# Optimization experiments

Hardware: AMD Instinct MI355X
Metric: run time of the kernel (lower is better)

## Reference

```python
import jax, jax.numpy as jnp
import numpy as np

D_K, D_V, H, N = 128, 256, 256, 50
B, L = 128, 1024

def setup_inputs() -> dict:
    key = jax.random.key(0)
    ks = jax.random.split(key, 10)
    s = lambda fan_in: 1.0 / np.sqrt(fan_in)
    return {
        'problems': jax.random.normal(ks[0], (B, L, D_K), dtype=jnp.float32),
        'interactions': jax.random.normal(ks[1], (B, L, D_V), dtype=jnp.float32),
        'w_key': jax.random.uniform(ks[2], (N, D_K), jnp.float32, -s(D_K), s(D_K)),
        'w_erase_w': jax.random.uniform(ks[3], (D_V, D_V), jnp.float32, -s(D_V), s(D_V)),
        'w_erase_b': jax.random.uniform(ks[4], (D_V,), jnp.float32, -s(D_V), s(D_V)),
        'w_add_w': jax.random.uniform(ks[5], (D_V, D_V), jnp.float32, -s(D_V), s(D_V)),
        'w_add_b': jax.random.uniform(ks[6], (D_V,), jnp.float32, -s(D_V), s(D_V)),
        'w_out_w': jax.random.uniform(ks[7], (H, D_V + D_K), jnp.float32, -s(D_V + D_K), s(D_V + D_K)),
        'w_out_b': jax.random.uniform(ks[8], (H,), jnp.float32, -s(D_V + D_K), s(D_V + D_K)),
        'init_memory': jax.random.normal(ks[9], (N, D_V), dtype=jnp.float32),
    }

def reference(problems, interactions, w_key, w_erase_w, w_erase_b, w_add_w, w_add_b, w_out_w, w_out_b, init_memory):
    # Precompute per-step gates outside the scan (they do not depend on memory)
    e = jax.nn.sigmoid(jnp.einsum('bld,ed->ble', interactions, w_erase_w) + w_erase_b)  # (B,L,d_v)
    a = jnp.tanh(jnp.einsum('bld,ed->ble', interactions, w_add_w) + w_add_b)            # (B,L,d_v)
    score = jax.nn.softmax(jnp.einsum('bld,nd->bln', problems, w_key), axis=-1)          # (B,L,n)

    mem0 = jnp.broadcast_to(init_memory, (problems.shape[0], N, D_V))

    def step(memory, xs):
        sc_t, e_t, a_t = xs  # (B,n), (B,d_v), (B,d_v)
        read = jnp.einsum('bn,bnd->bd', sc_t, memory)  # weighted read
        memory = memory * (1.0 - sc_t[:, :, None] * e_t[:, None, :])
        memory = memory + sc_t[:, :, None] * a_t[:, None, :]
        return memory, read

    xs = (score.transpose(1, 0, 2), e.transpose(1, 0, 2), a.transpose(1, 0, 2))  # time-major
    _, reads = jax.lax.scan(step, mem0, xs)  # reads: (L,B,d_v)

    x = jnp.concatenate([reads.transpose(1, 0, 2), problems], axis=-1)  # (B,L,d_v+d_k)
    # dropout in eval mode = identity
    return jnp.tanh(jnp.einsum('blc,hc->blh', x, w_out_w) + w_out_b)
```

## Files before the change

### kernel.cpp

```cpp
#include <hip/hip_runtime.h>

#define B_    128
#define L_    1024
#define DK_   128
#define DV_   256
#define NS_   50
#define H_    256
#define M_    (B_ * L_)

typedef __attribute__((ext_vector_type(8))) short   short8;
typedef __attribute__((ext_vector_type(4))) float   float4v;
typedef __attribute__((ext_vector_type(4))) int     int4v;

__device__ __forceinline__ float b2f(unsigned short u) {
    unsigned int x = ((unsigned int)u) << 16;
    return __builtin_bit_cast(float, x);
}
__device__ __forceinline__ unsigned short f2b(float f) {
    unsigned int x = __builtin_bit_cast(unsigned int, f);
    x += 0x7fffu + ((x >> 16) & 1u);
    return (unsigned short)(x >> 16);
}
__device__ __forceinline__ int pack2(float lo, float hi) {
    return (int)f2b(lo) | ((int)f2b(hi) << 16);
}
__device__ __forceinline__ float sigmoid_f(float x) {
    return 1.f / (1.f + __expf(-x));
}
__device__ __forceinline__ float tanh_f(float x) {
    return 1.f - 2.f / (__expf(2.f * x) + 1.f);
}

__device__ __forceinline__ void gload_lds16(const void* g, void* l) {
    __builtin_amdgcn_global_load_lds(
        (const __attribute__((address_space(1))) void*)g,
        (__attribute__((address_space(3))) void*)l, 16, 0, 0);
}

__global__ __launch_bounds__(256) void gate_kernel(
    const float* __restrict__ X,
    const float* __restrict__ We, const float* __restrict__ be,
    const float* __restrict__ Wa, const float* __restrict__ ba,
    unsigned short* __restrict__ e_out, unsigned short* __restrict__ a_out)
{
    constexpr int K = DV_;
    const int mblk = blockIdx.x, nblk = blockIdx.y, gate = blockIdx.z;
    const float* W    = gate ? Wa : We;
    const float* bias = gate ? ba : be;
    unsigned short* out = gate ? a_out : e_out;

    __shared__ unsigned short As[128 * 40];
    __shared__ unsigned short Bs[128 * 40];

    const int tid  = threadIdx.x;
    const int lane = tid & 63, wid = tid >> 6;
    const int wm = wid >> 1, wn = wid & 1;
    const int l15 = lane & 15, quad = lane >> 4;

    float4v acc[4][4];
#pragma unroll
    for (int i = 0; i < 4; i++)
#pragma unroll
        for (int j = 0; j < 4; j++) {
            acc[i][j][0] = 0.f; acc[i][j][1] = 0.f;
            acc[i][j][2] = 0.f; acc[i][j][3] = 0.f;
        }

    const int srow = tid >> 1;
    const int scol = (tid & 1) * 16;
    const size_t Abase = ((size_t)mblk * 128 + srow) * K;
    const size_t Bbase = ((size_t)nblk * 128 + srow) * K;

    for (int k0 = 0; k0 < K; k0 += 32) {
        const float* xa = &X[Abase + k0 + scol];
        const float* xb = &W[Bbase + k0 + scol];
        int4v pa0, pa1, pb0, pb1;
#pragma unroll
        for (int j = 0; j < 4; j++) {
            pa0[j] = pack2(xa[2*j],     xa[2*j + 1]);
            pa1[j] = pack2(xa[2*j + 8], xa[2*j + 9]);
            pb0[j] = pack2(xb[2*j],     xb[2*j + 1]);
            pb1[j] = pack2(xb[2*j + 8], xb[2*j + 9]);
        }
        *(int4v*)&As[srow * 40 + scol]     = pa0;
        *(int4v*)&As[srow * 40 + scol + 8] = pa1;
        *(int4v*)&Bs[srow * 40 + scol]     = pb0;
        *(int4v*)&Bs[srow * 40 + scol + 8] = pb1;
        __syncthreads();
        short8 af[4], bf[4];
#pragma unroll
        for (int i = 0; i < 4; i++)
            af[i] = *(const short8*)&As[(64 * wm + 16 * i + l15) * 40 + quad * 8];
#pragma unroll
        for (int j = 0; j < 4; j++)
            bf[j] = *(const short8*)&Bs[(64 * wn + 16 * j + l15) * 40 + quad * 8];
#pragma unroll
        for (int i = 0; i < 4; i++)
#pragma unroll
            for (int j = 0; j < 4; j++)
                acc[i][j] = __builtin_amdgcn_mfma_f32_16x16x32_bf16(af[i], bf[j], acc[i][j], 0, 0, 0);
        __syncthreads();
    }

#pragma unroll
    for (int i = 0; i < 4; i++) {
        const int row = mblk * 128 + 64 * wm + 16 * i + quad * 4;
#pragma unroll
        for (int j = 0; j < 4; j++) {
            const int col = nblk * 128 + 64 * wn + 16 * j + l15;
            const float bv = bias[col];
#pragma unroll
            for (int r = 0; r < 4; r++) {
                float v = acc[i][j][r] + bv;
                v = gate ? tanh_f(v) : sigmoid_f(v);
                out[(size_t)(row + r) * DV_ + col] = f2b(v);
            }
        }
    }
}

__global__ __launch_bounds__(256) void score_kernel(
    const float* __restrict__ problems,
    const float* __restrict__ w_key,
    float* __restrict__ score_scan)
{
    const int rowi = blockIdx.x * 256 + threadIdx.x;
    const float* p = problems + (size_t)rowi * DK_;

    float logit[NS_];
#pragma unroll
    for (int n = 0; n < NS_; n++) logit[n] = 0.f;

    for (int k0 = 0; k0 < DK_; k0 += 4) {
        float pf0 = p[k0], pf1 = p[k0+1], pf2 = p[k0+2], pf3 = p[k0+3];
#pragma unroll
        for (int n = 0; n < NS_; n++) {
            const float* wk = &w_key[n * DK_ + k0];
            logit[n] += pf0 * wk[0] + pf1 * wk[1] + pf2 * wk[2] + pf3 * wk[3];
        }
    }

    float mx = logit[0];
#pragma unroll
    for (int n = 1; n < NS_; n++) mx = fmaxf(mx, logit[n]);
    float sum = 0.f;
#pragma unroll
    for (int n = 0; n < NS_; n++) { logit[n] = __expf(logit[n] - mx); sum += logit[n]; }
    const float inv = 1.f / sum;

    float* o = score_scan + (size_t)rowi * 64;
#pragma unroll
    for (int v = 0; v < 16; v++) {
        float4v st;
#pragma unroll
        for (int c = 0; c < 4; c++) {
            const int j  = v * 4 + c;
            const int ng = j >> 4, ii = j & 15;
            const int n  = ng * 13 + ii;
            st[c] = (ii < 13 && n < NS_) ? logit[n] * inv : 0.f;
        }
        *(float4v*)(o + v * 4) = st;
    }
}

#define TCH 64
#define NCH (L_ / TCH)

__global__ __launch_bounds__(256) void scan_kernel(
    const float* __restrict__ score_scan,
    const unsigned short* __restrict__ e_buf,
    const unsigned short* __restrict__ a_buf,
    const float* __restrict__ init_mem,
    unsigned short* __restrict__ reads)
{
    __shared__ float          score_s[2][TCH][64];
    __shared__ unsigned short e_s[2][TCH][64];
    __shared__ unsigned short a_s[2][TCH][64];

    const int b    = blockIdx.y;
    const int dblk = blockIdx.x;
    const int tid  = threadIdx.x;
    const int w    = tid >> 6;
    const int lane = tid & 63;
    const int dsub = lane & 15;
    const int ng   = lane >> 4;
    const int d    = dblk * 64 + w * 16 + dsub;

    float M[13];
#pragma unroll
    for (int i = 0; i < 13; i++) {
        const int n = ng * 13 + i;
        M[i] = (n < NS_) ? init_mem[n * DV_ + d] : 0.f;
    }

    const size_t rb = (size_t)b * L_;
    const int l4  = lane >> 4;
    const int c16 = lane & 15;
    const int l8  = lane >> 3;
    const int c8  = lane & 7;

    auto stage = [&](int c, int p) {
        const int t0 = c * TCH + w * 16;
#pragma unroll
        for (int i = 0; i < 4; i++) {
            const int tt = t0 + i * 4 + l4;
            gload_lds16(score_scan + ((rb + tt) * 64 + c16 * 4),
                        &score_s[p][w * 16 + i * 4][0]);
        }
#pragma unroll
        for (int i = 0; i < 2; i++) {
            const int tt = t0 + i * 8 + l8;
            gload_lds16(e_buf + ((rb + tt) * DV_ + dblk * 64 + c8 * 8),
                        &e_s[p][w * 16 + i * 8][0]);
            gload_lds16(a_buf + ((rb + tt) * DV_ + dblk * 64 + c8 * 8),
                        &a_s[p][w * 16 + i * 8][0]);
        }
    };

    unsigned short* rp = reads + rb * DV_ + d;

    int p = 0;
    stage(0, 0);
    asm volatile("s_waitcnt vmcnt(0)" ::: "memory");
    __syncthreads();

    for (int c = 0; c < NCH; ++c) {
        if (c + 1 < NCH) stage(c + 1, p ^ 1);

#pragma unroll 2
        for (int tt = 0; tt < TCH; ++tt) {
            const float* sc = &score_s[p][tt][ng * 16];
            const float4v s0 = *(const float4v*)(sc);
            const float4v s1 = *(const float4v*)(sc + 4);
            const float4v s2 = *(const float4v*)(sc + 8);
            const float   s3 = sc[12];
            const float e_cur = b2f(e_s[p][tt][w * 16 + dsub]);
            const float a_cur = b2f(a_s[p][tt][w * 16 + dsub]);

            float r = 0.f;
            const float sarr[13] = { s0[0], s0[1], s0[2], s0[3],
                                     s1[0], s1[1], s1[2], s1[3],
                                     s2[0], s2[1], s2[2], s2[3], s3 };
#pragma unroll
            for (int i = 0; i < 13; i++) {
                const float s = sarr[i];
                r = fmaf(s, M[i], r);
                M[i] = fmaf(s, fmaf(-e_cur, M[i], a_cur), M[i]);
            }
            r += __shfl_xor(r, 16);
            r += __shfl_xor(r, 32);
            if (ng == 0) rp[(size_t)(c * TCH + tt) * DV_] = f2b(r);
        }

        asm volatile("s_waitcnt vmcnt(0)" ::: "memory");
        __syncthreads();
        p ^= 1;
    }
}

__global__ __launch_bounds__(256) void out_kernel(
    const unsigned short* __restrict__ reads,
    const float* __restrict__ problems,
    const float* __restrict__ Wo,
    const float* __restrict__ bo,
    float* __restrict__ out)
{
    constexpr int K = DV_ + DK_;
    const int mblk = blockIdx.x, nblk = blockIdx.y;

    __shared__ unsigned short As[128 * 40];
    __shared__ unsigned short Bs[128 * 40];

    const int tid  = threadIdx.x;
    const int lane = tid & 63, wid = tid >> 6;
    const int wm = wid >> 1, wn = wid & 1;
    const int l15 = lane & 15, quad = lane >> 4;

    float4v acc[4][4];
#pragma unroll
    for (int i = 0; i < 4; i++)
#pragma unroll
        for (int j = 0; j < 4; j++) {
            acc[i][j][0] = 0.f; acc[i][j][1] = 0.f;
            acc[i][j][2] = 0.f; acc[i][j][3] = 0.f;
        }

    const int srow = tid >> 1;
    const int scol = (tid & 1) * 16;
    const size_t mrow = (size_t)mblk * 128 + srow;
    const size_t brow = (size_t)nblk * 128 + srow;

    for (int k0 = 0; k0 < K; k0 += 32) {
        const int kk = k0 + scol;
        int4v a0, a1;
        if (kk < DV_) {
            a0 = *(const int4v*)&reads[mrow * DV_ + kk];
            a1 = *(const int4v*)&reads[mrow * DV_ + kk + 8];
        } else {
            const float* pr = &problems[mrow * DK_ + (kk - DV_)];
#pragma unroll
            for (int j = 0; j < 4; j++) {
                a0[j] = pack2(pr[2*j],     pr[2*j + 1]);
                a1[j] = pack2(pr[2*j + 8], pr[2*j + 9]);
            }
        }
        const float* wb = &Wo[brow * K + kk];
        int4v b0, b1;
#pragma unroll
        for (int j = 0; j < 4; j++) {
            b0[j] = pack2(wb[2*j],     wb[2*j + 1]);
            b1[j] = pack2(wb[2*j + 8], wb[2*j + 9]);
        }
        *(int4v*)&As[srow * 40 + scol]     = a0;
        *(int4v*)&As[srow * 40 + scol + 8] = a1;
        *(int4v*)&Bs[srow * 40 + scol]     = b0;
        *(int4v*)&Bs[srow * 40 + scol + 8] = b1;
        __syncthreads();
        short8 af[4], bf[4];
#pragma unroll
        for (int i = 0; i < 4; i++)
            af[i] = *(const short8*)&As[(64 * wm + 16 * i + l15) * 40 + quad * 8];
#pragma unroll
        for (int j = 0; j < 4; j++)
            bf[j] = *(const short8*)&Bs[(64 * wn + 16 * j + l15) * 40 + quad * 8];
#pragma unroll
        for (int i = 0; i < 4; i++)
#pragma unroll
            for (int j = 0; j < 4; j++)
                acc[i][j] = __builtin_amdgcn_mfma_f32_16x16x32_bf16(af[i], bf[j], acc[i][j], 0, 0, 0);
        __syncthreads();
    }

#pragma unroll
    for (int i = 0; i < 4; i++) {
        const int row = mblk * 128 + 64 * wm + 16 * i + quad * 4;
#pragma unroll
        for (int j = 0; j < 4; j++) {
            const int col = nblk * 128 + 64 * wn + 16 * j + l15;
            const float bv = bo[col];
#pragma unroll
            for (int r = 0; r < 4; r++) {
                out[(size_t)(row + r) * H_ + col] = tanh_f(acc[i][j][r] + bv);
            }
        }
    }
}

extern "C" void kernel_launch(void* const* d_in, const int* in_sizes, int n_in,
                              void* d_out, int out_size, void* d_ws, size_t ws_size,
                              hipStream_t stream) {
    const float* problems  = (const float*)d_in[0];
    const float* interact  = (const float*)d_in[1];
    const float* w_key     = (const float*)d_in[2];
    const float* w_erase_w = (const float*)d_in[3];
    const float* w_erase_b = (const float*)d_in[4];
    const float* w_add_w   = (const float*)d_in[5];
    const float* w_add_b   = (const float*)d_in[6];
    const float* w_out_w   = (const float*)d_in[7];
    const float* w_out_b   = (const float*)d_in[8];
    const float* init_mem  = (const float*)d_in[9];

    char* ws = (char*)d_ws;
    const size_t SZ_BF = (size_t)M_ * DV_ * 2;
    unsigned short* e_buf = (unsigned short*)(ws);
    unsigned short* a_buf = (unsigned short*)(ws + SZ_BF);
    unsigned short* reads = (unsigned short*)(ws + 2 * SZ_BF);
    float*     score_scan = (float*)(ws + 3 * SZ_BF);

    gate_kernel<<<dim3(M_ / 128, DV_ / 128, 2), 256, 0, stream>>>(
        interact, w_erase_w, w_erase_b, w_add_w, w_add_b, e_buf, a_buf);

    score_kernel<<<M_ / 256, 256, 0, stream>>>(problems, w_key, score_scan);

    scan_kernel<<<dim3(4, B_), 256, 0, stream>>>(
        score_scan, e_buf, a_buf, init_mem, reads);

    out_kernel<<<dim3(M_ / 128, H_ / 128), 256, 0, stream>>>(
        reads, problems, w_out_w, w_out_b, (float*)d_out);
}
```

Before: 838.3 us.

## Repartition scan across more blocks with 8 slots per lane group

The recurrent scan kernel now assigns 32 memory columns per block instead of 64, doubling the grid to 8x128 blocks, and splits the 50 memory slots into groups of 8 per lane (with an extra shuffle reduction) instead of 13. The score layout is changed to a contiguous 64-wide padded vector to match, the time chunk shrinks to 32 steps, and launch bounds request 4 blocks per CU. The GEMM kernels also switch from scalar float loads to float4 vector loads before bf16 packing. The aim is more parallelism and occupancy in the latency-bound sequential scan, at the cost of an extra cross-lane reduction and more redundant score loading per block.

```diff
diff --git a/kernel.cpp b/kernel.cpp
--- a/kernel.cpp
+++ b/kernel.cpp
@@ -74,14 +74,23 @@
     for (int k0 = 0; k0 < K; k0 += 32) {
         const float* xa = &X[Abase + k0 + scol];
         const float* xb = &W[Bbase + k0 + scol];
+        float4v va0 = *(const float4v*)(xa);
+        float4v va1 = *(const float4v*)(xa + 4);
+        float4v va2 = *(const float4v*)(xa + 8);
+        float4v va3 = *(const float4v*)(xa + 12);
+        float4v vb0 = *(const float4v*)(xb);
+        float4v vb1 = *(const float4v*)(xb + 4);
+        float4v vb2 = *(const float4v*)(xb + 8);
+        float4v vb3 = *(const float4v*)(xb + 12);
         int4v pa0, pa1, pb0, pb1;
-#pragma unroll
-        for (int j = 0; j < 4; j++) {
-            pa0[j] = pack2(xa[2*j],     xa[2*j + 1]);
-            pa1[j] = pack2(xa[2*j + 8], xa[2*j + 9]);
-            pb0[j] = pack2(xb[2*j],     xb[2*j + 1]);
-            pb1[j] = pack2(xb[2*j + 8], xb[2*j + 9]);
-        }
+        pa0[0] = pack2(va0[0], va0[1]); pa0[1] = pack2(va0[2], va0[3]);
+        pa0[2] = pack2(va1[0], va1[1]); pa0[3] = pack2(va1[2], va1[3]);
+        pa1[0] = pack2(va2[0], va2[1]); pa1[1] = pack2(va2[2], va2[3]);
+        pa1[2] = pack2(va3[0], va3[1]); pa1[3] = pack2(va3[2], va3[3]);
+        pb0[0] = pack2(vb0[0], vb0[1]); pb0[1] = pack2(vb0[2], vb0[3]);
+        pb0[2] = pack2(vb1[0], vb1[1]); pb0[3] = pack2(vb1[2], vb1[3]);
+        pb1[0] = pack2(vb2[0], vb2[1]); pb1[1] = pack2(vb2[2], vb2[3]);
+        pb1[2] = pack2(vb3[0], vb3[1]); pb1[3] = pack2(vb3[2], vb3[3]);
         *(int4v*)&As[srow * 40 + scol]     = pa0;
         *(int4v*)&As[srow * 40 + scol + 8] = pa1;
         *(int4v*)&Bs[srow * 40 + scol]     = pb0;
@@ -154,19 +163,17 @@
         float4v st;
 #pragma unroll
         for (int c = 0; c < 4; c++) {
-            const int j  = v * 4 + c;
-            const int ng = j >> 4, ii = j & 15;
-            const int n  = ng * 13 + ii;
-            st[c] = (ii < 13 && n < NS_) ? logit[n] * inv : 0.f;
+            const int j = v * 4 + c;
+            st[c] = (j < NS_) ? logit[j] * inv : 0.f;
         }
         *(float4v*)(o + v * 4) = st;
     }
 }
 
-#define TCH 64
+#define TCH 32
 #define NCH (L_ / TCH)
 
-__global__ __launch_bounds__(256) void scan_kernel(
+__global__ __launch_bounds__(256, 4) void scan_kernel(
     const float* __restrict__ score_scan,
     const unsigned short* __restrict__ e_buf,
     const unsigned short* __restrict__ a_buf,
@@ -174,46 +181,44 @@
     unsigned short* __restrict__ reads)
 {
     __shared__ float          score_s[2][TCH][64];
-    __shared__ unsigned short e_s[2][TCH][64];
-    __shared__ unsigned short a_s[2][TCH][64];
+    __shared__ unsigned short e_s[2][TCH][32];
+    __shared__ unsigned short a_s[2][TCH][32];
 
     const int b    = blockIdx.y;
     const int dblk = blockIdx.x;
     const int tid  = threadIdx.x;
     const int w    = tid >> 6;
     const int lane = tid & 63;
-    const int dsub = lane & 15;
-    const int ng   = lane >> 4;
-    const int d    = dblk * 64 + w * 16 + dsub;
-
-    float M[13];
-#pragma unroll
-    for (int i = 0; i < 13; i++) {
-        const int n = ng * 13 + i;
+    const int dsub = lane & 7;
+    const int ng   = lane >> 3;
+    const int dcol = w * 8 + dsub;
+    const int d    = dblk * 32 + dcol;
+
+    float M[8];
+#pragma unroll
+    for (int i = 0; i < 8; i++) {
+        const int n = ng * 8 + i;
         M[i] = (n < NS_) ? init_mem[n * DV_ + d] : 0.f;
     }
 
     const size_t rb = (size_t)b * L_;
-    const int l4  = lane >> 4;
-    const int c16 = lane & 15;
-    const int l8  = lane >> 3;
-    const int c8  = lane & 7;
 
     auto stage = [&](int c, int p) {
-        const int t0 = c * TCH + w * 16;
-#pragma unroll
-        for (int i = 0; i < 4; i++) {
-            const int tt = t0 + i * 4 + l4;
-            gload_lds16(score_scan + ((rb + tt) * 64 + c16 * 4),
-                        &score_s[p][w * 16 + i * 4][0]);
-        }
+        const int t0 = c * TCH;
 #pragma unroll
         for (int i = 0; i < 2; i++) {
-            const int tt = t0 + i * 8 + l8;
-            gload_lds16(e_buf + ((rb + tt) * DV_ + dblk * 64 + c8 * 8),
-                        &e_s[p][w * 16 + i * 8][0]);
-            gload_lds16(a_buf + ((rb + tt) * DV_ + dblk * 64 + c8 * 8),
-                        &a_s[p][w * 16 + i * 8][0]);
+            const int tt = t0 + w * 8 + i * 4 + (lane >> 4);
+            gload_lds16(score_scan + ((rb + tt) * 64 + (lane & 15) * 4),
+                        &score_s[p][w * 8 + i * 4][0]);
+        }
+        if (w < 2) {
+            const int tt = t0 + w * 16 + (lane >> 2);
+            gload_lds16(e_buf + ((rb + tt) * DV_ + dblk * 32 + (lane & 3) * 8),
+                        &e_s[p][w * 16][0]);
+        } else {
+            const int tt = t0 + (w - 2) * 16 + (lane >> 2);
+            gload_lds16(a_buf + ((rb + tt) * DV_ + dblk * 32 + (lane & 3) * 8),
+                        &a_s[p][(w - 2) * 16][0]);
         }
     };
 
@@ -227,26 +232,24 @@
     for (int c = 0; c < NCH; ++c) {
         if (c + 1 < NCH) stage(c + 1, p ^ 1);
 
-#pragma unroll 2
+#pragma unroll 4
         for (int tt = 0; tt < TCH; ++tt) {
-            const float* sc = &score_s[p][tt][ng * 16];
+            const float* sc = &score_s[p][tt][ng * 8];
             const float4v s0 = *(const float4v*)(sc);
             const float4v s1 = *(const float4v*)(sc + 4);
-            const float4v s2 = *(const float4v*)(sc + 8);
-            const float   s3 = sc[12];
-            const float e_cur = b2f(e_s[p][tt][w * 16 + dsub]);
-            const float a_cur = b2f(a_s[p][tt][w * 16 + dsub]);
+            const float e_cur = b2f(e_s[p][tt][dcol]);
+            const float a_cur = b2f(a_s[p][tt][dcol]);
 
             float r = 0.f;
-            const float sarr[13] = { s0[0], s0[1], s0[2], s0[3],
-                                     s1[0], s1[1], s1[2], s1[3],
-                                     s2[0], s2[1], s2[2], s2[3], s3 };
-#pragma unroll
-            for (int i = 0; i < 13; i++) {
+            const float sarr[8] = { s0[0], s0[1], s0[2], s0[3],
+                                    s1[0], s1[1], s1[2], s1[3] };
+#pragma unroll
+            for (int i = 0; i < 8; i++) {
                 const float s = sarr[i];
                 r = fmaf(s, M[i], r);
                 M[i] = fmaf(s, fmaf(-e_cur, M[i], a_cur), M[i]);
             }
+            r += __shfl_xor(r, 8);
             r += __shfl_xor(r, 16);
             r += __shfl_xor(r, 32);
             if (ng == 0) rp[(size_t)(c * TCH + tt) * DV_] = f2b(r);
@@ -298,19 +301,25 @@
             a1 = *(const int4v*)&reads[mrow * DV_ + kk + 8];
         } else {
             const float* pr = &problems[mrow * DK_ + (kk - DV_)];
-#pragma unroll
-            for (int j = 0; j < 4; j++) {
-                a0[j] = pack2(pr[2*j],     pr[2*j + 1]);
-                a1[j] = pack2(pr[2*j + 8], pr[2*j + 9]);
-            }
+            float4v v0 = *(const float4v*)(pr);
+            float4v v1 = *(const float4v*)(pr + 4);
+            float4v v2 = *(const float4v*)(pr + 8);
+            float4v v3 = *(const float4v*)(pr + 12);
+            a0[0] = pack2(v0[0], v0[1]); a0[1] = pack2(v0[2], v0[3]);
+            a0[2] = pack2(v1[0], v1[1]); a0[3] = pack2(v1[2], v1[3]);
+            a1[0] = pack2(v2[0], v2[1]); a1[1] = pack2(v2[2], v2[3]);
+            a1[2] = pack2(v3[0], v3[1]); a1[3] = pack2(v3[2], v3[3]);
         }
         const float* wb = &Wo[brow * K + kk];
+        float4v u0 = *(const float4v*)(wb);
+        float4v u1 = *(const float4v*)(wb + 4);
+        float4v u2 = *(const float4v*)(wb + 8);
+        float4v u3 = *(const float4v*)(wb + 12);
         int4v b0, b1;
-#pragma unroll
-        for (int j = 0; j < 4; j++) {
-            b0[j] = pack2(wb[2*j],     wb[2*j + 1]);
-            b1[j] = pack2(wb[2*j + 8], wb[2*j + 9]);
-        }
+        b0[0] = pack2(u0[0], u0[1]); b0[1] = pack2(u0[2], u0[3]);
+        b0[2] = pack2(u1[0], u1[1]); b0[3] = pack2(u1[2], u1[3]);
+        b1[0] = pack2(u2[0], u2[1]); b1[1] = pack2(u2[2], u2[3]);
+        b1[2] = pack2(u3[0], u3[1]); b1[3] = pack2(u3[2], u3[3]);
         *(int4v*)&As[srow * 40 + scol]     = a0;
         *(int4v*)&As[srow * 40 + scol + 8] = a1;
         *(int4v*)&Bs[srow * 40 + scol]     = b0;
@@ -372,7 +381,7 @@
 
     score_kernel<<<M_ / 256, 256, 0, stream>>>(problems, w_key, score_scan);
 
-    scan_kernel<<<dim3(4, B_), 256, 0, stream>>>(
+    scan_kernel<<<dim3(8, B_), 256, 0, stream>>>(
         score_scan, e_buf, a_buf, init_mem, reads);
 
     out_kernel<<<dim3(M_ / 128, H_ / 128), 256, 0, stream>>>(
```

After: 870.2 us. 3.8% more time.
